# Performance work log

Hardware: AMD Instinct MI355X
Metric: run time of the kernel (lower is better)

The kernel has to match this reference:

```python
import jax, jax.numpy as jnp
import numpy as np

N = 50000      # nodes
E = 800000     # edges
D = 128        # hidden dim (args.dim) == num_features
B = 5          # GIN blocks
G = 512        # graphs in batch
C = 10         # classes
EPS_GIN = 128.0  # GINConv(nn, in_channels) -> eps = in_channels = 128 (faithful to source)
BN_EPS = 1e-5


def setup_inputs() -> dict:
    key = jax.random.key(0)
    ks = jax.random.split(key, 12)
    xav = 0.1  # ~xavier_uniform std for 128x128
    x = jax.random.normal(ks[0], (N, D), jnp.float32)
    edge_index = jax.random.randint(ks[1], (2, E), 0, N, dtype=jnp.int64)
    batch = jax.random.randint(ks[2], (N,), 0, G, dtype=jnp.int64)
    return dict(
        x=x, edge_index=edge_index, batch=batch,
        W1=jax.random.normal(ks[3], (B, D, D), jnp.float32) * xav,
        b1=jnp.zeros((B, D), jnp.float32),
        g1=jnp.ones((B, D), jnp.float32),
        be1=jnp.zeros((B, D), jnp.float32),
        W2=jax.random.normal(ks[4], (B, D, D), jnp.float32) * xav,
        b2=jnp.zeros((B, D), jnp.float32),
        g2=jnp.ones((B, D), jnp.float32),
        be2=jnp.zeros((B, D), jnp.float32),
        bn_g=jnp.ones((B * D,), jnp.float32),
        bn_b=jnp.zeros((B * D,), jnp.float32),
        Wc1=jax.random.normal(ks[5], (B * D, D), jnp.float32) * 0.05,
        bc1=jnp.zeros((D,), jnp.float32),
        Wc2=jax.random.normal(ks[6], (D, C), jnp.float32) * 0.1,
        bc2=jnp.zeros((C,), jnp.float32),
    )


def _bn(h, g, b):
    # training-mode BatchNorm1d: biased variance over the batch (node/graph) dim
    mu = h.mean(axis=0)
    var = h.var(axis=0)
    return g * (h - mu) * jax.lax.rsqrt(var + BN_EPS) + b


def reference(x, edge_index, batch, W1, b1, g1, be1, W2, b2, g2, be2,
              bn_g, bn_b, Wc1, bc1, Wc2, bc2):
    src, dst = edge_index[0], edge_index[1]
    feats = []
    for i in range(B):
        # GIN aggregation: out[dst] += x[src]
        agg = jax.ops.segment_sum(x[src], dst, num_segments=N)   # [N, D]
        h = (1.0 + EPS_GIN) * x + agg
        h = _bn(jax.nn.relu(h @ W1[i] + b1[i]), g1[i], be1[i])
        h = _bn(jax.nn.relu(h @ W2[i] + b2[i]), g2[i], be2[i])
        x = h
        # global_add_pool per graph
        feats.append(jax.ops.segment_sum(x, batch, num_segments=G))  # [G, D]
    f = jnp.concatenate(feats, axis=1)          # [G, B*D]
    f = _bn(f, bn_g, bn_b)
    f = jax.nn.relu(f @ Wc1 + bc1)              # dropout p=0 (eval)
    logits = f @ Wc2 + bc2                      # [G, C]
    return jax.nn.log_softmax(logits, axis=-1)
```

## Files before the change

kernel.cpp:

```cpp
#include <hip/hip_runtime.h>
#include <hip/hip_bf16.h>

#define NN 50000
#define NE 800000
#define DD 128
#define NB 5
#define NG 512
#define NC 10
#define BN_EPS 1e-5f
#define EPS1 129.0f
#define GATHER_BLOCKS 12500

typedef __hip_bfloat16 bf16;
typedef __attribute__((ext_vector_type(8))) short short8;
typedef __attribute__((ext_vector_type(4))) float f32x4;

__device__ __forceinline__ float b2f(const bf16 v) { return __bfloat162float(v); }
__device__ __forceinline__ float us2f(unsigned int s) {
    return __uint_as_float((s & 0xffffu) << 16);
}
__device__ __forceinline__ unsigned pack2(float a, float b) {
    union { bf16 h; unsigned short u; } ua, ub;
    ua.h = __float2bfloat16(a); ub.h = __float2bfloat16(b);
    return ((unsigned)ub.u << 16) | (unsigned)ua.u;
}
__device__ __forceinline__ short f2bfs(float f) {
    union { bf16 h; short s; } u; u.h = __float2bfloat16(f); return u.s;
}

#define OFF_AGGH   0
#define OFF_XF     3200000
#define OFF_H1     6400000
#define OFF_FEATS  9600000
#define OFF_CSA    9927680
#define OFF_CSB    9927936
#define OFF_SC6    9928192
#define OFF_SH6    9928832
#define OFF_FLAGS  9929472
#define OFF_PARAMS 9929480
#define OFF_DEG    10055680
#define OFF_OFFS   10105680
#define OFF_ELIST  10155712
#define OFF_BDEG   10955712
#define OFF_BOFFS  10956224
#define OFF_RANK   10956800
#define OFF_PART   11006800
#define OFF_ERANK  11006864

#define P_W1T  0
#define P_W2T  81920
#define P_WC1  163840
#define P_B1   245760
#define P_G1   246400
#define P_BE1  247040
#define P_B2   247680
#define P_G2   248320
#define P_BE2  248960
#define P_BNG  249600
#define P_BNB  250240
#define P_BC1  250880
#define P_WC2  251008
#define P_BC2  252288

struct SmallSrc { const void* s[11]; };

__global__ void k_detect(const unsigned* __restrict__ xw, const int* __restrict__ eiw,
                         const int* __restrict__ bw, int* flags, int* __restrict__ bdeg) {
    __shared__ int sh[3];
    const int t = threadIdx.x;
    bdeg[t] = 0; bdeg[256 + t] = 0;
    if (t < 3) sh[t] = 0;
    __syncthreads();
    int c = 0;
    for (int i = 0; i < 16; i++) {
        unsigned w = xw[t * 16 + i];
        unsigned e = (w >> 7) & 0xff;
        c += (e >= 110 && e <= 131) ? 1 : 0;
    }
    atomicAdd(&sh[0], c);
    atomicAdd(&sh[1], (eiw[2 * t + 1] != 0) ? 1 : 0);
    atomicAdd(&sh[2], (bw[2 * t + 1] != 0) ? 1 : 0);
    __syncthreads();
    if (t == 0) {
        flags[0] = (sh[0] > 2048) ? 1 : 0;
        flags[1] = (sh[1] < 8) ? 1 : 0;
        flags[2] = (sh[2] < 8) ? 1 : 0;
    }
}

__global__ void k_bhist(const int* __restrict__ flags, const int* __restrict__ batch,
                        int* __restrict__ bdeg, int* __restrict__ deg) {
    int n = blockIdx.x * 256 + threadIdx.x;
    if (n >= NN) return;
    deg[n] = 0;
    int g = flags[2] ? batch[2 * n] : batch[n];
    atomicAdd(&bdeg[g], 1);
}

__launch_bounds__(512)
__global__ void k_bscan(int* __restrict__ bdeg, int* __restrict__ boffs) {
    __shared__ int part[512];
    const int t = threadIdx.x;
    int d0 = bdeg[t];
    part[t] = d0;
    __syncthreads();
    for (int d = 1; d < 512; d <<= 1) {
        int v = (t >= d) ? part[t - d] : 0;
        __syncthreads();
        part[t] += v;
        __syncthreads();
    }
    int ex = part[t] - d0;
    boffs[t] = ex;
    bdeg[t] = ex;
    if (t == 511) boffs[512] = part[511];
}

__global__ void k_bplace(const int* __restrict__ flags, const int* __restrict__ batch,
                         int* __restrict__ bcur, int* __restrict__ rank) {
    int n = blockIdx.x * 256 + threadIdx.x;
    if (n >= NN) return;
    int g = flags[2] ? batch[2 * n] : batch[n];
    rank[n] = atomicAdd(&bcur[g], 1);
}

__global__ void k_convert_x(const int* __restrict__ flags, const void* __restrict__ xr,
                            const int* __restrict__ rank, bf16* __restrict__ xfh) {
    int i = blockIdx.x * 256 + threadIdx.x;
    int r = i >> 4, seg = i & 15;
    uint4 o;
    if (flags[0]) {
        o = ((const uint4*)xr)[i];
    } else {
        float4 a = ((const float4*)xr)[2 * i], b = ((const float4*)xr)[2 * i + 1];
        o.x = pack2(a.x, a.y); o.y = pack2(a.z, a.w);
        o.z = pack2(b.x, b.y); o.w = pack2(b.z, b.w);
    }
    ((uint4*)xfh)[(long)rank[r] * 16 + seg] = o;
}

__global__ void k_convert_params(const int* __restrict__ flags, const void* w1,
                                 const void* w2, const void* wc1, SmallSrc srcs,
                                 bf16* __restrict__ pb) {
    int i = blockIdx.x * 256 + threadIdx.x;
    if (i < 245760) {
        int which = i / 81920, j = i % 81920;
        const void* src = (which == 0) ? w1 : (which == 1) ? w2 : wc1;
        float v = flags[0] ? us2f(((const unsigned short*)src)[j]) : ((const float*)src)[j];
        if (which == 2) {
            int rowj = j >> 7, col = j & 127;
            pb[P_WC1 + col * (NB * DD) + rowj] = __float2bfloat16(v);
        } else {
            int layer = j >> 14, rem = j & 16383;
            int k = rem >> 7, c = rem & 127;
            bf16* dst = pb + (which == 0 ? P_W1T : P_W2T);
            dst[(layer << 14) + c * DD + k] = __float2bfloat16(v);
        }
    } else {
        int j = i - 245760;
        if (j >= 6538) return;
        int seg, off;
        if (j < 5120)      { seg = j / 640; off = j - seg * 640; }
        else if (j < 5248) { seg = 8;  off = j - 5120; }
        else if (j < 6528) { seg = 9;  off = j - 5248; }
        else               { seg = 10; off = j - 6528; }
        const void* s = srcs.s[seg];
        float v = flags[0] ? us2f(((const unsigned short*)s)[off]) : ((const float*)s)[off];
        pb[P_B1 + j] = __float2bfloat16(v);
    }
}

__global__ void k_hist(const int* __restrict__ flags, const int* __restrict__ ei,
                       const int* __restrict__ rank, int* __restrict__ deg,
                       int* __restrict__ erank) {
    int e = blockIdx.x * 256 + threadIdx.x;
    int d = flags[1] ? ei[2 * NE + 2 * e] : ei[NE + e];
    erank[e] = atomicAdd(&deg[rank[d]], 1);
}

__global__ void k_scan_part(const int* __restrict__ deg, int* __restrict__ part) {
    __shared__ int red[256];
    const int b = blockIdx.x, t = threadIdx.x;
    int i0 = b * 1024 + t * 4;
    int s = 0;
    if (i0 + 3 < NN) {
        int4 v = *(const int4*)(deg + i0);
        s = v.x + v.y + v.z + v.w;
    } else {
        for (int k = 0; k < 4; k++) if (i0 + k < NN) s += deg[i0 + k];
    }
    red[t] = s;
    __syncthreads();
    for (int d = 128; d > 0; d >>= 1) {
        if (t < d) red[t] += red[t + d];
        __syncthreads();
    }
    if (t == 0) part[b] = red[0];
}

__global__ void k_scan_apply(const int* __restrict__ deg, const int* __restrict__ part,
                             int* __restrict__ offs) {
    __shared__ int red[256];
    __shared__ int base_sh, total_sh;
    const int b = blockIdx.x, t = threadIdx.x;
    if (t < 64) {
        int v = (t < 49) ? part[t] : 0;
        int s = v;
        for (int d = 1; d < 64; d <<= 1) {
            int x = __shfl_up(s, d);
            if (t >= d) s += x;
        }
        if (t == b)  base_sh = s - v;
        if (t == 48) total_sh = s;
    }
    int i0 = b * 1024 + t * 4;
    int v[4]; int s = 0;
    #pragma unroll
    for (int k = 0; k < 4; k++) {
        int idx = i0 + k;
        v[k] = (idx < NN) ? deg[idx] : 0;
        s += v[k];
    }
    red[t] = s;
    __syncthreads();
    for (int d = 1; d < 256; d <<= 1) {
        int x = (t >= d) ? red[t - d] : 0;
        __syncthreads();
        red[t] += x;
        __syncthreads();
    }
    if (b == 0 && t == 0) offs[NN] = total_sh;
    int pre = base_sh + ((t == 0) ? 0 : red[t - 1]);
    #pragma unroll
    for (int k = 0; k < 4; k++) {
        int idx = i0 + k;
        if (idx < NN) { offs[idx] = pre; pre += v[k]; }
    }
}

__global__ void k_place(const int* __restrict__ flags, const int* __restrict__ ei,
                        const int* __restrict__ rank, const int* __restrict__ offs,
                        const int* __restrict__ erank, int* __restrict__ elist) {
    int e = blockIdx.x * 256 + threadIdx.x;
    int s, d;
    if (flags[1]) { s = ei[2 * e]; d = ei[2 * NE + 2 * e]; }
    else          { s = ei[e];     d = ei[NE + e]; }
    elist[offs[rank[d]] + erank[e]] = rank[s];
}

__device__ __forceinline__ void pool_body(int g, int t, const bf16* __restrict__ xfh,
                                          const int* __restrict__ boffs,
                                          const float* __restrict__ csB,
                                          const bf16* __restrict__ g2,
                                          const bf16* __restrict__ be2,
                                          float* __restrict__ feats_blk) {
    __shared__ float2 red[3][64];
    const int l = t & 63;
    const int h = t >> 6;
    const int lo = boffs[g], hi = boffs[g + 1];
    const unsigned* xw = (const unsigned*)xfh;
    float s0 = 0.f, s1 = 0.f;
    for (int n = lo + h; n < hi; n += 4) {
        unsigned p = xw[(long)n * 64 + l];
        s0 += us2f(p); s1 += us2f(p >> 16);
    }
    if (h) red[h - 1][l] = make_float2(s0, s1);
    __syncthreads();
    if (h == 0) {
        s0 += red[0][l].x + red[1][l].x + red[2][l].x;
        s1 += red[0][l].y + red[1][l].y + red[2][l].y;
        int c = l * 2;
        float mu0 = csB[c] * (1.f / NN);
        float var0 = csB[128 + c] * (1.f / NN) - mu0 * mu0;
        float sc0 = b2f(g2[c]) * rsqrtf(var0 + BN_EPS);
        float sh0 = b2f(be2[c]) - mu0 * sc0;
        float mu1 = csB[c + 1] * (1.f / NN);
        float var1 = csB[128 + c + 1] * (1.f / NN) - mu1 * mu1;
        float sc1 = b2f(g2[c + 1]) * rsqrtf(var1 + BN_EPS);
        float sh1 = b2f(be2[c + 1]) - mu1 * sc1;
        float cnt = (float)(hi - lo);
        float* fp = feats_blk + (long)g * (NB * DD) + c;
        fp[0] = sc0 * s0 + cnt * sh0;
        fp[1] = sc1 * s1 + cnt * sh1;
    }
}

__global__ void k_gather_pool(const int* __restrict__ offs, const int* __restrict__ elist,
                              const bf16* __restrict__ xfh, bf16* __restrict__ aggh,
                              const float* __restrict__ csB, const bf16* __restrict__ g2,
                              const bf16* __restrict__ be2, float* __restrict__ csA_zero,
                              const int* __restrict__ boffs, float* __restrict__ feats_prev) {
    if (blockIdx.x >= GATHER_BLOCKS) {
        if (feats_prev)
            pool_body(blockIdx.x - GATHER_BLOCKS, threadIdx.x, xfh, boffs,
                      csB, g2, be2, feats_prev);
        return;
    }
    if (blockIdx.x == 0) csA_zero[threadIdx.x] = 0.f;
    const int w = threadIdx.x >> 6;
    const int lane = threadIdx.x & 63;
    const int half = lane >> 5;
    const int ql = lane & 31;
    const int n = blockIdx.x * 4 + w;
    const int base = offs[n], end = offs[n + 1];
    const uint2* xw2 = (const uint2*)xfh;

    float a0, a1, a2, a3;
    {
        uint2 sp = xw2[(long)n * 32 + ql];
        float m = (half == 0) ? EPS1 : 0.f;
        a0 = m * us2f(sp.x); a1 = m * us2f(sp.x >> 16);
        a2 = m * us2f(sp.y); a3 = m * us2f(sp.y >> 16);
    }

    for (int i = base; i < end; i += 64) {
        int cnt = min(64, end - i);
        int e = (i + lane < end) ? elist[i + lane] : 0;
        int j = 0;
        for (; j + 16 <= cnt; j += 16) {
            uint2 p[8];
            #pragma unroll
            for (int q = 0; q < 8; q++) {
                int sj = __shfl(e, j + 2 * q + half);
                p[q] = xw2[(long)sj * 32 + ql];
            }
            #pragma unroll
            for (int q = 0; q < 8; q++) {
                a0 += us2f(p[q].x); a1 += us2f(p[q].x >> 16);
                a2 += us2f(p[q].y); a3 += us2f(p[q].y >> 16);
            }
        }
        for (; j + 2 <= cnt; j += 2) {
            int sj = __shfl(e, j + half);
            uint2 p = xw2[(long)sj * 32 + ql];
            a0 += us2f(p.x); a1 += us2f(p.x >> 16);
            a2 += us2f(p.y); a3 += us2f(p.y >> 16);
        }
        if (j < cnt && half == 0) {
            int sj = __shfl(e, j);
            uint2 p = xw2[(long)sj * 32 + ql];
            a0 += us2f(p.x); a1 += us2f(p.x >> 16);
            a2 += us2f(p.y); a3 += us2f(p.y >> 16);
        }
    }
    a0 += __shfl_xor(a0, 32); a1 += __shfl_xor(a1, 32);
    a2 += __shfl_xor(a2, 32); a3 += __shfl_xor(a3, 32);

    if (csB) {
        int c = ql * 4;
        float fac = (float)(end - base) + EPS1;
        #pragma unroll
        for (int k = 0; k < 4; k++) {
            float mu = csB[c + k] * (1.f / NN);
            float var = csB[128 + c + k] * (1.f / NN) - mu * mu;
            float sc = b2f(g2[c + k]) * rsqrtf(var + BN_EPS);
            float sh = b2f(be2[c + k]) - mu * sc;
            float* ap = (k == 0) ? &a0 : (k == 1) ? &a1 : (k == 2) ? &a2 : &a3;
            *ap = sc * (*ap) + fac * sh;
        }
    }
    if (half == 0)
        ((uint2*)aggh)[(long)n * 32 + ql] = make_uint2(pack2(a0, a1), pack2(a2, a3));
}

__launch_bounds__(256)
__global__ void k_pool(const bf16* __restrict__ xfh, const int* __restrict__ boffs,
                       const float* __restrict__ csB, const bf16* __restrict__ g2,
                       const bf16* __restrict__ be2, float* __restrict__ feats_blk) {
    pool_body(blockIdx.x, threadIdx.x, xfh, boffs, csB, g2, be2, feats_blk);
}

#define WS_S 136
__launch_bounds__(512)
__global__ void k_gemm_mfma(const bf16* __restrict__ A, const bf16* __restrict__ WT,
                            const bf16* __restrict__ bias,
                            const float* __restrict__ bn_cs, const bf16* __restrict__ bn_g,
                            const bf16* __restrict__ bn_be,
                            bf16* __restrict__ Out, float* __restrict__ cs_out,
                            float* cs_zero) {
    __shared__ short Ws[128 * WS_S];
    __shared__ float s_cs[256];
    __shared__ float s_sc[DD], s_sh[DD];
    const int t = threadIdx.x;
    const int row0 = blockIdx.x * 128;

    if (t < 256) {
        if (cs_zero && blockIdx.x == 0) cs_zero[t] = 0.f;
        s_cs[t] = 0.f;
    }
    if (bn_cs && t < DD) {
        float mu = bn_cs[t] * (1.f / NN);
        float var = bn_cs[128 + t] * (1.f / NN) - mu * mu;
        float sc = b2f(bn_g[t]) * rsqrtf(var + BN_EPS);
        s_sc[t] = sc;
        s_sh[t] = b2f(bn_be[t]) - mu * sc;
    }
    {
        const uint4* Wg = (const uint4*)WT;
        #pragma unroll
        for (int i = 0; i < 4; i++) {
            int idx = i * 512 + t;
            int row = idx >> 4, seg = idx & 15;
            *(uint4*)(&Ws[row * WS_S + seg * 8]) = Wg[idx];
        }
    }
    __syncthreads();

    const int w = t >> 6;
    const int lane = t & 63;
    const int m = lane & 15;
    const int half = lane >> 4;
    const int r = row0 + w * 16 + m;

    short8 afrag[4];
    if (r < NN) {
        #pragma unroll
        for (int kk = 0; kk < 4; kk++)
            afrag[kk] = *(const short8*)(A + (long)r * DD + kk * 32 + half * 8);
        if (bn_cs) {
            #pragma unroll
            for (int kk = 0; kk < 4; kk++) {
                int c0 = kk * 32 + half * 8;
                uint4 p = *(uint4*)&afrag[kk];
                float v0 = us2f(p.x) * s_sc[c0+0] + s_sh[c0+0];
                float v1 = us2f(p.x >> 16) * s_sc[c0+1] + s_sh[c0+1];
                float v2 = us2f(p.y) * s_sc[c0+2] + s_sh[c0+2];
                float v3 = us2f(p.y >> 16) * s_sc[c0+3] + s_sh[c0+3];
                float v4 = us2f(p.z) * s_sc[c0+4] + s_sh[c0+4];
                float v5 = us2f(p.z >> 16) * s_sc[c0+5] + s_sh[c0+5];
                float v6 = us2f(p.w) * s_sc[c0+6] + s_sh[c0+6];
                float v7 = us2f(p.w >> 16) * s_sc[c0+7] + s_sh[c0+7];
                p.x = pack2(v0, v1); p.y = pack2(v2, v3);
                p.z = pack2(v4, v5); p.w = pack2(v6, v7);
                afrag[kk] = *(short8*)&p;
            }
        }
    } else {
        #pragma unroll
        for (int kk = 0; kk < 4; kk++) afrag[kk] = (short8){0,0,0,0,0,0,0,0};
    }

    f32x4 acc[8];
    #pragma unroll
    for (int nt = 0; nt < 8; nt++) acc[nt] = (f32x4){0.f, 0.f, 0.f, 0.f};

    #pragma unroll
    for (int nt = 0; nt < 8; nt++) {
        const short* wrow = &Ws[(nt * 16 + m) * WS_S + half * 8];
        #pragma unroll
        for (int kk = 0; kk < 4; kk++) {
            short8 b = *(const short8*)(wrow + kk * 32);
            acc[nt] = __builtin_amdgcn_mfma_f32_16x16x32_bf16(afrag[kk], b, acc[nt], 0, 0, 0);
        }
    }

    __syncthreads();
    short* Cs = Ws;
    #pragma unroll
    for (int nt = 0; nt < 8; nt++) {
        int col = nt * 16 + m;
        float bi = b2f(bias[col]);
        float ps = 0.f, pq = 0.f;
        #pragma unroll
        for (int reg = 0; reg < 4; reg++) {
            int rr = row0 + w * 16 + half * 4 + reg;
            float o = fmaxf(acc[nt][reg] + bi, 0.f);
            Cs[(w * 16 + half * 4 + reg) * WS_S + col] = f2bfs(o);
            if (rr < NN) { ps += o; pq += o * o; }
        }
        ps += __shfl_xor(ps, 16); ps += __shfl_xor(ps, 32);
        pq += __shfl_xor(pq, 16); pq += __shfl_xor(pq, 32);
        if (half == 0) {
            atomicAdd(&s_cs[col], ps);
            atomicAdd(&s_cs[128 + col], pq);
        }
    }
    __syncthreads();
    #pragma unroll
    for (int i = 0; i < 4; i++) {
        int idx = i * 512 + t;
        int row = idx >> 4, seg = idx & 15;
        int rr = row0 + row;
        if (rr < NN)
            *(uint4*)(Out + (long)rr * DD + seg * 8) = *(uint4*)(&Cs[row * WS_S + seg * 8]);
    }
    if (t < 256) atomicAdd(&cs_out[t], s_cs[t]);
}

__launch_bounds__(256)
__global__ void k_feat_stats(const float* __restrict__ feats, const bf16* __restrict__ bn_g,
                             const bf16* __restrict__ bn_b, float* __restrict__ sc6,
                             float* __restrict__ sh6) {
    __shared__ float rs[8][32], rq[8][32];
    const int j0 = blockIdx.x * 32;
    const int jl = threadIdx.x & 31, gg = threadIdx.x >> 5;
    float s = 0.f, q = 0.f;
    for (int g = gg; g < NG; g += 8) {
        float v = feats[(long)g * (NB * DD) + j0 + jl];
        s += v; q += v * v;
    }
    rs[gg][jl] = s; rq[gg][jl] = q;
    __syncthreads();
    if (gg == 0) {
        #pragma unroll
        for (int k = 1; k < 8; k++) { s += rs[k][jl]; q += rq[k][jl]; }
        int j = j0 + jl;
        float mu = s / NG;
        float var = q / NG - mu * mu;
        float sc = b2f(bn_g[j]) * rsqrtf(var + BN_EPS);
        sc6[j] = sc;
        sh6[j] = b2f(bn_b[j]) - mu * sc;
    }
}

__launch_bounds__(128)
__global__ void k_head(const int* __restrict__ flags, const float* __restrict__ feats,
                       const float* __restrict__ sc6, const float* __restrict__ sh6,
                       const bf16* __restrict__ Wc1T, const bf16* __restrict__ bc1,
                       const bf16* __restrict__ Wc2, const bf16* __restrict__ bc2,
                       void* out) {
    __shared__ float fs[NB * DD];
    __shared__ float f1[DD];
    __shared__ float lg[NC + 2];
    const int g = blockIdx.x, t = threadIdx.x;
    for (int j = t; j < NB * DD; j += 128)
        fs[j] = feats[(long)g * (NB * DD) + j] * sc6[j] + sh6[j];
    __syncthreads();
    float acc = b2f(bc1[t]);
    {
        const short8* wr = (const short8*)(Wc1T + (long)t * (NB * DD));
        #pragma unroll 4
        for (int jb = 0; jb < 80; jb++) {
            short8 wv = wr[jb];
            uint4 p = *(uint4*)&wv;
            float4 f0 = *(const float4*)&fs[jb * 8];
            float4 f1v = *(const float4*)&fs[jb * 8 + 4];
            acc += f0.x * us2f(p.x) + f0.y * us2f(p.x >> 16)
                 + f0.z * us2f(p.y) + f0.w * us2f(p.y >> 16)
                 + f1v.x * us2f(p.z) + f1v.y * us2f(p.z >> 16)
                 + f1v.z * us2f(p.w) + f1v.w * us2f(p.w >> 16);
        }
    }
    f1[t] = fmaxf(acc, 0.f);
    __syncthreads();
    if (t < NC) {
        float a = b2f(bc2[t]);
        for (int k = 0; k < DD; k++) a += f1[k] * b2f(Wc2[k * NC + t]);
        lg[t] = a;
    }
    __syncthreads();
    if (t == 0) {
        float m = -1e30f;
        for (int c = 0; c < NC; c++) m = fmaxf(m, lg[c]);
        float s = 0.f;
        for (int c = 0; c < NC; c++) s += expf(lg[c] - m);
        lg[NC] = m + logf(s);
    }
    __syncthreads();
    if (t < NC) {
        float val = lg[t] - lg[NC];
        if (flags[0]) ((bf16*)out)[g * NC + t] = __float2bfloat16(val);
        else          ((float*)out)[g * NC + t] = val;
    }
}

extern "C" void kernel_launch(void* const* d_in, const int* in_sizes, int n_in,
                              void* d_out, int out_size, void* d_ws, size_t ws_size,
                              hipStream_t stream) {
    const void* x     = d_in[0];
    const int*  ei    = (const int*)d_in[1];
    const int*  batch = (const int*)d_in[2];

    float* ws    = (float*)d_ws;
    bf16*  aggh  = (bf16*)(ws + OFF_AGGH);
    bf16*  xfh   = (bf16*)(ws + OFF_XF);
    bf16*  h1h   = (bf16*)(ws + OFF_H1);
    float* feats = ws + OFF_FEATS;
    float* csA   = ws + OFF_CSA;
    float* csB   = ws + OFF_CSB;
    float* sc6   = ws + OFF_SC6;
    float* sh6   = ws + OFF_SH6;
    int*   flags = (int*)(ws + OFF_FLAGS);
    bf16*  pb    = (bf16*)(ws + OFF_PARAMS);
    int*   deg   = (int*)(ws + OFF_DEG);
    int*   offs  = (int*)(ws + OFF_OFFS);
    int*   elist = (int*)(ws + OFF_ELIST);
    int*   bdeg  = (int*)(ws + OFF_BDEG);
    int*   boffs = (int*)(ws + OFF_BOFFS);
    int*   rank  = (int*)(ws + OFF_RANK);
    int*   part  = (int*)(ws + OFF_PART);
    int*   erank = (int*)(ws + OFF_ERANK);

    bf16 *pW1T = pb + P_W1T, *pW2T = pb + P_W2T, *pWc1 = pb + P_WC1;
    bf16 *pb1 = pb + P_B1, *pg1 = pb + P_G1, *pbe1 = pb + P_BE1;
    bf16 *pb2 = pb + P_B2, *pg2 = pb + P_G2, *pbe2 = pb + P_BE2;
    bf16 *pbng = pb + P_BNG, *pbnb = pb + P_BNB;
    bf16 *pbc1 = pb + P_BC1, *pWc2 = pb + P_WC2, *pbc2 = pb + P_BC2;

    k_detect<<<1, 256, 0, stream>>>((const unsigned*)x, ei, batch, flags, bdeg);

    k_bhist<<<(NN + 255) / 256, 256, 0, stream>>>(flags, batch, bdeg, deg);
    k_bscan<<<1, 512, 0, stream>>>(bdeg, boffs);
    k_bplace<<<(NN + 255) / 256, 256, 0, stream>>>(flags, batch, bdeg, rank);

    k_convert_x<<<NN * DD / 8 / 256, 256, 0, stream>>>(flags, x, rank, xfh);

    SmallSrc ss;
    ss.s[0] = d_in[4];  ss.s[1] = d_in[5];  ss.s[2] = d_in[6];
    ss.s[3] = d_in[8];  ss.s[4] = d_in[9];  ss.s[5] = d_in[10];
    ss.s[6] = d_in[11]; ss.s[7] = d_in[12];
    ss.s[8] = d_in[14]; ss.s[9] = d_in[15]; ss.s[10] = d_in[16];
    k_convert_params<<<(245760 + 6538 + 255) / 256, 256, 0, stream>>>(
        flags, d_in[3], d_in[7], d_in[13], ss, pb);

    k_hist<<<NE / 256, 256, 0, stream>>>(flags, ei, rank, deg, erank);
    k_scan_part<<<49, 256, 0, stream>>>(deg, part);
    k_scan_apply<<<49, 256, 0, stream>>>(deg, part, offs);
    k_place<<<NE / 256, 256, 0, stream>>>(flags, ei, rank, offs, erank, elist);

    const int gemm_blocks = (NN + 127) / 128;
    for (int i = 0; i < NB; i++) {
        k_gather_pool<<<GATHER_BLOCKS + NG, 256, 0, stream>>>(
            offs, elist, xfh, aggh,
            (i == 0) ? nullptr : csB,
            pg2 + (i - 1) * DD, pbe2 + (i - 1) * DD, csA,
            boffs, (i == 0) ? nullptr : feats + (i - 1) * DD);
        k_gemm_mfma<<<gemm_blocks, 512, 0, stream>>>(aggh, pW1T + i * DD * DD, pb1 + i * DD,
                                                     nullptr, nullptr, nullptr,
                                                     h1h, csA, csB);
        k_gemm_mfma<<<gemm_blocks, 512, 0, stream>>>(h1h, pW2T + i * DD * DD, pb2 + i * DD,
                                                     csA, pg1 + i * DD, pbe1 + i * DD,
                                                     xfh, csB, nullptr);
    }
    k_pool<<<NG, 256, 0, stream>>>(xfh, boffs, csB, pg2 + (NB - 1) * DD,
                                   pbe2 + (NB - 1) * DD, feats + (NB - 1) * DD);

    k_feat_stats<<<20, 256, 0, stream>>>(feats, pbng, pbnb, sc6, sh6);
    k_head<<<NG, 128, 0, stream>>>(flags, feats, sc6, sh6, pWc1, pbc1, pWc2, pbc2, d_out);
}
```

Measured before the change: 645.7 us.

## Fuse neighbor gather into first GEMM and double-buffer BN stat buffers

Merges the edge-gather aggregation kernel with the first MFMA GEMM, so each 512-thread block gathers 128 node rows into shared memory and multiplies them by W1 right away. This removes the bf16 aggregation buffer round trip through global memory and one kernel launch per layer. The pooling blocks stay piggybacked on the same launch, now with 8 waves each. Column-stat buffers are double-buffered so the zeroing of the next layer's stats can be folded into existing kernels. The trade-off is only 391 gather blocks instead of 12500, which cuts the parallelism available to hide the irregular gather latency. It also adds large shared-memory use per block, which may lower occupancy.

```diff
diff --git a/kernel.cpp b/kernel.cpp
--- a/kernel.cpp
+++ b/kernel.cpp
@@ -9,7 +9,7 @@
 #define NC 10
 #define BN_EPS 1e-5f
 #define EPS1 129.0f
-#define GATHER_BLOCKS 12500
+#define GEMM_BLOCKS 391
 
 typedef __hip_bfloat16 bf16;
 typedef __attribute__((ext_vector_type(8))) short short8;
@@ -46,6 +46,7 @@
 #define OFF_RANK   10956800
 #define OFF_PART   11006800
 #define OFF_ERANK  11006864
+#define OFF_CS2    11806864
 
 #define P_W1T  0
 #define P_W2T  81920
@@ -240,7 +241,9 @@
 
 __global__ void k_place(const int* __restrict__ flags, const int* __restrict__ ei,
                         const int* __restrict__ rank, const int* __restrict__ offs,
-                        const int* __restrict__ erank, int* __restrict__ elist) {
+                        const int* __restrict__ erank, int* __restrict__ elist,
+                        float* __restrict__ csA0) {
+    if (blockIdx.x == 0) csA0[threadIdx.x] = 0.f;
     int e = blockIdx.x * 256 + threadIdx.x;
     int s, d;
     if (flags[1]) { s = ei[2 * e]; d = ei[2 * NE + 2 * e]; }
@@ -248,27 +251,28 @@
     elist[offs[rank[d]] + erank[e]] = rank[s];
 }
 
+template<int NH>
 __device__ __forceinline__ void pool_body(int g, int t, const bf16* __restrict__ xfh,
                                           const int* __restrict__ boffs,
                                           const float* __restrict__ csB,
                                           const bf16* __restrict__ g2,
                                           const bf16* __restrict__ be2,
                                           float* __restrict__ feats_blk) {
-    __shared__ float2 red[3][64];
+    __shared__ float2 red[NH - 1][64];
     const int l = t & 63;
     const int h = t >> 6;
     const int lo = boffs[g], hi = boffs[g + 1];
     const unsigned* xw = (const unsigned*)xfh;
     float s0 = 0.f, s1 = 0.f;
-    for (int n = lo + h; n < hi; n += 4) {
+    for (int n = lo + h; n < hi; n += NH) {
         unsigned p = xw[(long)n * 64 + l];
         s0 += us2f(p); s1 += us2f(p >> 16);
     }
     if (h) red[h - 1][l] = make_float2(s0, s1);
     __syncthreads();
     if (h == 0) {
-        s0 += red[0][l].x + red[1][l].x + red[2][l].x;
-        s1 += red[0][l].y + red[1][l].y + red[2][l].y;
+        #pragma unroll
+        for (int k = 0; k < NH - 1; k++) { s0 += red[k][l].x; s1 += red[k][l].y; }
         int c = l * 2;
         float mu0 = csB[c] * (1.f / NN);
         float var0 = csB[128 + c] * (1.f / NN) - mu0 * mu0;
@@ -285,92 +289,176 @@
     }
 }
 
-__global__ void k_gather_pool(const int* __restrict__ offs, const int* __restrict__ elist,
-                              const bf16* __restrict__ xfh, bf16* __restrict__ aggh,
-                              const float* __restrict__ csB, const bf16* __restrict__ g2,
-                              const bf16* __restrict__ be2, float* __restrict__ csA_zero,
-                              const int* __restrict__ boffs, float* __restrict__ feats_prev) {
-    if (blockIdx.x >= GATHER_BLOCKS) {
+#define WS_S 136
+__launch_bounds__(512, 4)
+__global__ void k_gather_gemm1(const int* __restrict__ offs, const int* __restrict__ elist,
+                               const bf16* __restrict__ xfh,
+                               const float* __restrict__ csBp,
+                               const bf16* __restrict__ g2, const bf16* __restrict__ be2,
+                               const bf16* __restrict__ W1T, const bf16* __restrict__ b1v,
+                               bf16* __restrict__ Out, float* __restrict__ csA_out,
+                               float* __restrict__ csB_zero,
+                               const int* __restrict__ boffs, float* __restrict__ feats_prev) {
+    if (blockIdx.x >= GEMM_BLOCKS) {
         if (feats_prev)
-            pool_body(blockIdx.x - GATHER_BLOCKS, threadIdx.x, xfh, boffs,
-                      csB, g2, be2, feats_prev);
+            pool_body<8>(blockIdx.x - GEMM_BLOCKS, threadIdx.x, xfh, boffs,
+                         csBp, g2, be2, feats_prev);
         return;
     }
-    if (blockIdx.x == 0) csA_zero[threadIdx.x] = 0.f;
-    const int w = threadIdx.x >> 6;
-    const int lane = threadIdx.x & 63;
+    __shared__ short Ws[128 * WS_S];
+    __shared__ short As[128 * WS_S];
+    __shared__ float s_cs[256];
+    const int t = threadIdx.x;
+    const int row0 = blockIdx.x * 128;
+
+    if (t < 256) {
+        s_cs[t] = 0.f;
+        if (blockIdx.x == 0) csB_zero[t] = 0.f;
+    }
+    {
+        const uint4* Wg = (const uint4*)W1T;
+        #pragma unroll
+        for (int i = 0; i < 4; i++) {
+            int idx = i * 512 + t;
+            *(uint4*)(&Ws[(idx >> 4) * WS_S + (idx & 15) * 8]) = Wg[idx];
+        }
+    }
+
+    const int w = t >> 6;
+    const int lane = t & 63;
     const int half = lane >> 5;
     const int ql = lane & 31;
-    const int n = blockIdx.x * 4 + w;
-    const int base = offs[n], end = offs[n + 1];
     const uint2* xw2 = (const uint2*)xfh;
 
-    float a0, a1, a2, a3;
-    {
-        uint2 sp = xw2[(long)n * 32 + ql];
-        float m = (half == 0) ? EPS1 : 0.f;
-        a0 = m * us2f(sp.x); a1 = m * us2f(sp.x >> 16);
-        a2 = m * us2f(sp.y); a3 = m * us2f(sp.y >> 16);
-    }
-
-    for (int i = base; i < end; i += 64) {
-        int cnt = min(64, end - i);
-        int e = (i + lane < end) ? elist[i + lane] : 0;
-        int j = 0;
-        for (; j + 16 <= cnt; j += 16) {
-            uint2 p[8];
-            #pragma unroll
-            for (int q = 0; q < 8; q++) {
-                int sj = __shfl(e, j + 2 * q + half);
-                p[q] = xw2[(long)sj * 32 + ql];
+    float bsc[4], bsh[4];
+    if (csBp) {
+        int c = ql * 4;
+        #pragma unroll
+        for (int k = 0; k < 4; k++) {
+            float mu = csBp[c + k] * (1.f / NN);
+            float var = csBp[128 + c + k] * (1.f / NN) - mu * mu;
+            bsc[k] = b2f(g2[c + k]) * rsqrtf(var + BN_EPS);
+            bsh[k] = b2f(be2[c + k]) - mu * bsc[k];
+        }
+    }
+
+    for (int k = 0; k < 16; k++) {
+        const int n = row0 + w * 16 + k;
+        float a0 = 0.f, a1 = 0.f, a2 = 0.f, a3 = 0.f;
+        if (n < NN) {
+            const int base = offs[n], end = offs[n + 1];
+            {
+                uint2 sp = xw2[(long)n * 32 + ql];
+                float m = (half == 0) ? EPS1 : 0.f;
+                a0 = m * us2f(sp.x); a1 = m * us2f(sp.x >> 16);
+                a2 = m * us2f(sp.y); a3 = m * us2f(sp.y >> 16);
             }
-            #pragma unroll
-            for (int q = 0; q < 8; q++) {
-                a0 += us2f(p[q].x); a1 += us2f(p[q].x >> 16);
-                a2 += us2f(p[q].y); a3 += us2f(p[q].y >> 16);
+            for (int i = base; i < end; i += 64) {
+                int cnt = min(64, end - i);
+                int e = (i + lane < end) ? elist[i + lane] : 0;
+                int j = 0;
+                for (; j + 16 <= cnt; j += 16) {
+                    uint2 p[8];
+                    #pragma unroll
+                    for (int q = 0; q < 8; q++) {
+                        int sj = __shfl(e, j + 2 * q + half);
+                        p[q] = xw2[(long)sj * 32 + ql];
+                    }
+                    #pragma unroll
+                    for (int q = 0; q < 8; q++) {
+                        a0 += us2f(p[q].x); a1 += us2f(p[q].x >> 16);
+                        a2 += us2f(p[q].y); a3 += us2f(p[q].y >> 16);
+                    }
+                }
+                for (; j + 2 <= cnt; j += 2) {
+                    int sj = __shfl(e, j + half);
+                    uint2 p = xw2[(long)sj * 32 + ql];
+                    a0 += us2f(p.x); a1 += us2f(p.x >> 16);
+                    a2 += us2f(p.y); a3 += us2f(p.y >> 16);
+                }
+                if (j < cnt && half == 0) {
+                    int sj = __shfl(e, j);
+                    uint2 p = xw2[(long)sj * 32 + ql];
+                    a0 += us2f(p.x); a1 += us2f(p.x >> 16);
+                    a2 += us2f(p.y); a3 += us2f(p.y >> 16);
+                }
             }
-        }
-        for (; j + 2 <= cnt; j += 2) {
-            int sj = __shfl(e, j + half);
-            uint2 p = xw2[(long)sj * 32 + ql];
-            a0 += us2f(p.x); a1 += us2f(p.x >> 16);
-            a2 += us2f(p.y); a3 += us2f(p.y >> 16);
-        }
-        if (j < cnt && half == 0) {
-            int sj = __shfl(e, j);
-            uint2 p = xw2[(long)sj * 32 + ql];
-            a0 += us2f(p.x); a1 += us2f(p.x >> 16);
-            a2 += us2f(p.y); a3 += us2f(p.y >> 16);
-        }
-    }
-    a0 += __shfl_xor(a0, 32); a1 += __shfl_xor(a1, 32);
-    a2 += __shfl_xor(a2, 32); a3 += __shfl_xor(a3, 32);
-
-    if (csB) {
-        int c = ql * 4;
-        float fac = (float)(end - base) + EPS1;
-        #pragma unroll
-        for (int k = 0; k < 4; k++) {
-            float mu = csB[c + k] * (1.f / NN);
-            float var = csB[128 + c + k] * (1.f / NN) - mu * mu;
-            float sc = b2f(g2[c + k]) * rsqrtf(var + BN_EPS);
-            float sh = b2f(be2[c + k]) - mu * sc;
-            float* ap = (k == 0) ? &a0 : (k == 1) ? &a1 : (k == 2) ? &a2 : &a3;
-            *ap = sc * (*ap) + fac * sh;
-        }
-    }
-    if (half == 0)
-        ((uint2*)aggh)[(long)n * 32 + ql] = make_uint2(pack2(a0, a1), pack2(a2, a3));
+            a0 += __shfl_xor(a0, 32); a1 += __shfl_xor(a1, 32);
+            a2 += __shfl_xor(a2, 32); a3 += __shfl_xor(a3, 32);
+            if (csBp) {
+                float fac = (float)(end - base) + EPS1;
+                a0 = bsc[0] * a0 + fac * bsh[0];
+                a1 = bsc[1] * a1 + fac * bsh[1];
+                a2 = bsc[2] * a2 + fac * bsh[2];
+                a3 = bsc[3] * a3 + fac * bsh[3];
+            }
+        }
+        if (half == 0)
+            *(uint2*)(&As[(w * 16 + k) * WS_S + ql * 4]) =
+                make_uint2(pack2(a0, a1), pack2(a2, a3));
+    }
+    __syncthreads();
+
+    const int m = lane & 15;
+    const int mh = lane >> 4;
+    short8 afrag[4];
+    #pragma unroll
+    for (int kk = 0; kk < 4; kk++)
+        afrag[kk] = *(const short8*)(&As[(w * 16 + m) * WS_S + kk * 32 + mh * 8]);
+
+    f32x4 acc[8];
+    #pragma unroll
+    for (int nt = 0; nt < 8; nt++) acc[nt] = (f32x4){0.f, 0.f, 0.f, 0.f};
+    #pragma unroll
+    for (int nt = 0; nt < 8; nt++) {
+        const short* wrow = &Ws[(nt * 16 + m) * WS_S + mh * 8];
+        #pragma unroll
+        for (int kk = 0; kk < 4; kk++) {
+            short8 b = *(const short8*)(wrow + kk * 32);
+            acc[nt] = __builtin_amdgcn_mfma_f32_16x16x32_bf16(afrag[kk], b, acc[nt], 0, 0, 0);
+        }
+    }
+
+    __syncthreads();
+    short* Cs = Ws;
+    #pragma unroll
+    for (int nt = 0; nt < 8; nt++) {
+        int col = nt * 16 + m;
+        float bi = b2f(b1v[col]);
+        float ps = 0.f, pq = 0.f;
+        #pragma unroll
+        for (int reg = 0; reg < 4; reg++) {
+            int rr = row0 + w * 16 + mh * 4 + reg;
+            float o = fmaxf(acc[nt][reg] + bi, 0.f);
+            Cs[(w * 16 + mh * 4 + reg) * WS_S + col] = f2bfs(o);
+            if (rr < NN) { ps += o; pq += o * o; }
+        }
+        ps += __shfl_xor(ps, 16); ps += __shfl_xor(ps, 32);
+        pq += __shfl_xor(pq, 16); pq += __shfl_xor(pq, 32);
+        if (mh == 0) {
+            atomicAdd(&s_cs[col], ps);
+            atomicAdd(&s_cs[128 + col], pq);
+        }
+    }
+    __syncthreads();
+    #pragma unroll
+    for (int i = 0; i < 4; i++) {
+        int idx = i * 512 + t;
+        int row = idx >> 4, seg = idx & 15;
+        int rr = row0 + row;
+        if (rr < NN)
+            *(uint4*)(Out + (long)rr * DD + seg * 8) = *(uint4*)(&Cs[row * WS_S + seg * 8]);
+    }
+    if (t < 256) atomicAdd(&csA_out[t], s_cs[t]);
 }
 
 __launch_bounds__(256)
 __global__ void k_pool(const bf16* __restrict__ xfh, const int* __restrict__ boffs,
                        const float* __restrict__ csB, const bf16* __restrict__ g2,
                        const bf16* __restrict__ be2, float* __restrict__ feats_blk) {
-    pool_body(blockIdx.x, threadIdx.x, xfh, boffs, csB, g2, be2, feats_blk);
-}
-
-#define WS_S 136
+    pool_body<4>(blockIdx.x, threadIdx.x, xfh, boffs, csB, g2, be2, feats_blk);
+}
+
 __launch_bounds__(512)
 __global__ void k_gemm_mfma(const bf16* __restrict__ A, const bf16* __restrict__ WT,
                             const bf16* __restrict__ bias,
@@ -572,12 +660,9 @@
     const int*  batch = (const int*)d_in[2];
 
     float* ws    = (float*)d_ws;
-    bf16*  aggh  = (bf16*)(ws + OFF_AGGH);
     bf16*  xfh   = (bf16*)(ws + OFF_XF);
     bf16*  h1h   = (bf16*)(ws + OFF_H1);
     float* feats = ws + OFF_FEATS;
-    float* csA   = ws + OFF_CSA;
-    float* csB   = ws + OFF_CSB;
     float* sc6   = ws + OFF_SC6;
     float* sh6   = ws + OFF_SH6;
     int*   flags = (int*)(ws + OFF_FLAGS);
@@ -591,6 +676,9 @@
     int*   part  = (int*)(ws + OFF_PART);
     int*   erank = (int*)(ws + OFF_ERANK);
 
+    float* csA_buf[2] = { ws + OFF_CSA, ws + OFF_CS2 };
+    float* csB_buf[2] = { ws + OFF_CSB, ws + OFF_CS2 + 256 };
+
     bf16 *pW1T = pb + P_W1T, *pW2T = pb + P_W2T, *pWc1 = pb + P_WC1;
     bf16 *pb1 = pb + P_B1, *pg1 = pb + P_G1, *pbe1 = pb + P_BE1;
     bf16 *pb2 = pb + P_B2, *pg2 = pb + P_G2, *pbe2 = pb + P_BE2;
@@ -616,24 +704,26 @@
     k_hist<<<NE / 256, 256, 0, stream>>>(flags, ei, rank, deg, erank);
     k_scan_part<<<49, 256, 0, stream>>>(deg, part);
     k_scan_apply<<<49, 256, 0, stream>>>(deg, part, offs);
-    k_place<<<NE / 256, 256, 0, stream>>>(flags, ei, rank, offs, erank, elist);
-
-    const int gemm_blocks = (NN + 127) / 128;
+    k_place<<<NE / 256, 256, 0, stream>>>(flags, ei, rank, offs, erank, elist,
+                                          csA_buf[0]);
+
     for (int i = 0; i < NB; i++) {
-        k_gather_pool<<<GATHER_BLOCKS + NG, 256, 0, stream>>>(
-            offs, elist, xfh, aggh,
-            (i == 0) ? nullptr : csB,
-            pg2 + (i - 1) * DD, pbe2 + (i - 1) * DD, csA,
+        k_gather_gemm1<<<GEMM_BLOCKS + NG, 512, 0, stream>>>(
+            offs, elist, xfh,
+            (i == 0) ? nullptr : csB_buf[(i - 1) & 1],
+            pg2 + (i - 1) * DD, pbe2 + (i - 1) * DD,
+            pW1T + i * DD * DD, pb1 + i * DD,
+            h1h, csA_buf[i & 1], csB_buf[i & 1],
             boffs, (i == 0) ? nullptr : feats + (i - 1) * DD);
-        k_gemm_mfma<<<gemm_blocks, 512, 0, stream>>>(aggh, pW1T + i * DD * DD, pb1 + i * DD,
-                                                     nullptr, nullptr, nullptr,
-                                                     h1h, csA, csB);
-        k_gemm_mfma<<<gemm_blocks, 512, 0, stream>>>(h1h, pW2T + i * DD * DD, pb2 + i * DD,
-                                                     csA, pg1 + i * DD, pbe1 + i * DD,
-                                                     xfh, csB, nullptr);
-    }
-    k_pool<<<NG, 256, 0, stream>>>(xfh, boffs, csB, pg2 + (NB - 1) * DD,
-                                   pbe2 + (NB - 1) * DD, feats + (NB - 1) * DD);
+        k_gemm_mfma<<<GEMM_BLOCKS, 512, 0, stream>>>(
+            h1h, pW2T + i * DD * DD, pb2 + i * DD,
+            csA_buf[i & 1], pg1 + i * DD, pbe1 + i * DD,
+            xfh, csB_buf[i & 1],
+            (i < NB - 1) ? csA_buf[(i + 1) & 1] : nullptr);
+    }
+    k_pool<<<NG, 256, 0, stream>>>(xfh, boffs, csB_buf[(NB - 1) & 1],
+                                   pg2 + (NB - 1) * DD, pbe2 + (NB - 1) * DD,
+                                   feats + (NB - 1) * DD);
 
     k_feat_stats<<<20, 256, 0, stream>>>(feats, pbng, pbnb, sc6, sh6);
     k_head<<<NG, 128, 0, stream>>>(flags, feats, sc6, sh6, pWc1, pbc1, pWc2, pbc2, d_out);
```

Result: slower. 689.0 us (+6.7%).
